# Optimization experiments

Hardware: AMD Instinct MI355X
Metric: run time of the kernel (lower is better)

## Reference

```python
import jax, jax.numpy as jnp
import numpy as np

DIM = 1024
B = 65536


def setup_inputs() -> dict:
    key = jax.random.key(0)
    k1, k2, k3 = jax.random.split(key, 3)
    x_l = jax.random.normal(k1, (B, DIM), dtype=jnp.float32)
    x_0 = jax.random.normal(k2, (B, DIM), dtype=jnp.float32)
    # xavier_uniform for w of shape (dim, 1): bound = sqrt(6/(dim+1))
    bound = float(np.sqrt(6.0 / (DIM + 1)))
    w = jax.random.uniform(k3, (DIM, 1), dtype=jnp.float32, minval=-bound, maxval=bound)
    b = jnp.zeros((DIM, 1), dtype=jnp.float32)
    return {"x_l": x_l, "x_0": x_0, "w": w, "b": b}


def reference(x_l, x_0, w, b):
    # Original: (x_0 @ x_l^T) @ w + b + x_l  (per-example outer product).
    # By associativity: x_0 * (x_l . w) + b + x_l, avoiding the B x dim x dim intermediate.
    s = x_l @ w                      # [B, 1] == x_l . w per example
    out = x_0 * s + b[:, 0] + x_l    # broadcast bias over batch
    return out
```

## Files before the change

kernel.cpp:

```cpp
#include <hip/hip_runtime.h>
#include <hip/hip_bf16.h>


#define DIM 1024
#define BLOCK 256

__global__ __launch_bounds__(BLOCK) void dcn_fused_kernel(
    const float* __restrict__ x_l,
    const float* __restrict__ x_0,
    const float* __restrict__ w,
    const float* __restrict__ b,
    float* __restrict__ out)
{
    const int row = blockIdx.x;
    const int tid = threadIdx.x;
    const size_t base = (size_t)row * DIM + (size_t)tid * 4;
    const int col = tid * 4;

    const float4 xl = *(const float4*)(x_l + base);
    const float4 wv = *(const float4*)(w + col);

    float partial = xl.x * wv.x + xl.y * wv.y + xl.z * wv.z + xl.w * wv.w;

    #pragma unroll
    for (int off = 32; off > 0; off >>= 1)
        partial += __shfl_down(partial, off, 64);

    __shared__ float wsum[4];
    const int wave = tid >> 6;
    const int lane = tid & 63;
    if (lane == 0) wsum[wave] = partial;
    __syncthreads();
    const float s = wsum[0] + wsum[1] + wsum[2] + wsum[3];

    const float4 x0 = *(const float4*)(x_0 + base);
    const float4 bv = *(const float4*)(b + col);

    float4 o;
    o.x = fmaf(x0.x, s, bv.x + xl.x);
    o.y = fmaf(x0.y, s, bv.y + xl.y);
    o.z = fmaf(x0.z, s, bv.z + xl.z);
    o.w = fmaf(x0.w, s, bv.w + xl.w);

    *(float4*)(out + base) = o;
}

extern "C" void kernel_launch(void* const* d_in, const int* in_sizes, int n_in,
                              void* d_out, int out_size, void* d_ws, size_t ws_size,
                              hipStream_t stream) {
    const float* x_l = (const float*)d_in[0];
    const float* x_0 = (const float*)d_in[1];
    const float* w   = (const float*)d_in[2];
    const float* b   = (const float*)d_in[3];
    float* out = (float*)d_out;

    const int B = in_sizes[0] / DIM;
    dcn_fused_kernel<<<B, BLOCK, 0, stream>>>(x_l, x_0, w, b, out);
}
```

Measured before the change: 566.2 us.

## Map one row per wavefront and prefetch all row loads before reduction

Each wavefront now processes a whole row, so the block-level shared-memory reduction and barrier are replaced by a wave-wide xor shuffle reduction. All x_l, x_0, w and b loads for the row are issued up front, raising the number of memory requests in flight before the dot-product dependency. The grid shrinks by four and register use per thread grows.

```diff
diff --git a/kernel.cpp b/kernel.cpp
--- a/kernel.cpp
+++ b/kernel.cpp
@@ -1,5 +1,4 @@
 #include <hip/hip_runtime.h>
-#include <hip/hip_bf16.h>
 
 
 #define DIM 1024
@@ -12,37 +11,49 @@
     const float* __restrict__ b,
     float* __restrict__ out)
 {
-    const int row = blockIdx.x;
-    const int tid = threadIdx.x;
-    const size_t base = (size_t)row * DIM + (size_t)tid * 4;
-    const int col = tid * 4;
+    const int wave = threadIdx.x >> 6;
+    const int lane = threadIdx.x & 63;
+    const int row  = blockIdx.x * 4 + wave;
+    const size_t rowbase = (size_t)row * DIM;
+    const int c0 = lane * 4;
 
-    const float4 xl = *(const float4*)(x_l + base);
-    const float4 wv = *(const float4*)(w + col);
+    float4 xl[4], x0[4], wv[4], bv[4];
+    #pragma unroll
+    for (int k = 0; k < 4; ++k)
+        xl[k] = *(const float4*)(x_l + rowbase + k * 256 + c0);
+    #pragma unroll
+    for (int k = 0; k < 4; ++k)
+        x0[k] = *(const float4*)(x_0 + rowbase + k * 256 + c0);
+    #pragma unroll
+    for (int k = 0; k < 4; ++k)
+        wv[k] = *(const float4*)(w + k * 256 + c0);
+    #pragma unroll
+    for (int k = 0; k < 4; ++k)
+        bv[k] = *(const float4*)(b + k * 256 + c0);
 
-    float partial = xl.x * wv.x + xl.y * wv.y + xl.z * wv.z + xl.w * wv.w;
+    float partial = 0.0f;
+    #pragma unroll
+    for (int k = 0; k < 4; ++k) {
+        partial = fmaf(xl[k].x, wv[k].x, partial);
+        partial = fmaf(xl[k].y, wv[k].y, partial);
+        partial = fmaf(xl[k].z, wv[k].z, partial);
+        partial = fmaf(xl[k].w, wv[k].w, partial);
+    }
 
     #pragma unroll
-    for (int off = 32; off > 0; off >>= 1)
-        partial += __shfl_down(partial, off, 64);
+    for (int off = 1; off < 64; off <<= 1)
+        partial += __shfl_xor(partial, off, 64);
+    const float s = partial;
 
-    __shared__ float wsum[4];
-    const int wave = tid >> 6;
-    const int lane = tid & 63;
-    if (lane == 0) wsum[wave] = partial;
-    __syncthreads();
-    const float s = wsum[0] + wsum[1] + wsum[2] + wsum[3];
-
-    const float4 x0 = *(const float4*)(x_0 + base);
-    const float4 bv = *(const float4*)(b + col);
-
-    float4 o;
-    o.x = fmaf(x0.x, s, bv.x + xl.x);
-    o.y = fmaf(x0.y, s, bv.y + xl.y);
-    o.z = fmaf(x0.z, s, bv.z + xl.z);
-    o.w = fmaf(x0.w, s, bv.w + xl.w);
-
-    *(float4*)(out + base) = o;
+    #pragma unroll
+    for (int k = 0; k < 4; ++k) {
+        float4 o;
+        o.x = fmaf(x0[k].x, s, bv[k].x + xl[k].x);
+        o.y = fmaf(x0[k].y, s, bv[k].y + xl[k].y);
+        o.z = fmaf(x0[k].z, s, bv[k].z + xl[k].z);
+        o.w = fmaf(x0[k].w, s, bv[k].w + xl[k].w);
+        *(float4*)(out + rowbase + k * 256 + c0) = o;
+    }
 }
 
 extern "C" void kernel_launch(void* const* d_in, const int* in_sizes, int n_in,
@@ -55,5 +66,5 @@
     float* out = (float*)d_out;
 
     const int B = in_sizes[0] / DIM;
-    dcn_fused_kernel<<<B, BLOCK, 0, stream>>>(x_l, x_0, w, b, out);
+    dcn_fused_kernel<<<B / 4, BLOCK, 0, stream>>>(x_l, x_0, w, b, out);
 }
```

Measured after the change: 572.6 us. Within noise of the previous version (+1.1%).
